# Optimization experiments

Measured on AMD Instinct MI355X. Metric: run time of the kernel, lower is better.

The kernel has to match this reference:

```python
import jax, jax.numpy as jnp
import numpy as np

B, N, D = 32, 4096, 1024

def setup_inputs() -> dict:
    key = jax.random.key(0)
    k1, k2, k3, k4 = jax.random.split(key, 4)
    return {
        "x_final": jax.random.normal(k1, (B, D), dtype=jnp.float32),
        "x_full": jax.random.normal(k2, (B, N, D), dtype=jnp.float32),
        "mask": jnp.ones((B, N), dtype=bool),
        "q": jax.random.normal(k3, (D,), dtype=jnp.float32) / np.sqrt(D),
        "head_w": jax.random.normal(k4, (1, D), dtype=jnp.float32) / np.sqrt(D),
        "head_b": jnp.zeros((1,), dtype=jnp.float32),
    }

def reference(x_final, x_full, mask, q, head_w, head_b):
    # x_final is accepted (as in the torch module) but unused.
    d = x_full.shape[-1]
    inv_sqrt_d = 1.0 / np.sqrt(d)
    # logits: [B, N] = matvec of x_full with learned query q
    logits = jnp.einsum('bnd,d->bn', x_full, q) * inv_sqrt_d
    logits = jnp.where(mask, logits, -jnp.inf)
    alpha = jax.nn.softmax(logits, axis=-1)          # [B, N]
    pooled = jnp.einsum('bn,bnd->bd', alpha, x_full) # [B, D]
    scores = (pooled @ head_w.T + head_b)[:, 0]      # [B]
    return scores, alpha
```

## Files before the change

### kernel.cpp

```cpp
#include <hip/hip_runtime.h>
#include <math.h>

#define B_ 32
#define N_ 4096
#define D_ 1024
#define ROWS (B_ * N_)

#define P1_BLOCKS 2048
#define P1_THREADS 256
#define NWAVES (P1_BLOCKS * (P1_THREADS / 64))
#define ROWS_PER_WAVE (ROWS / NWAVES)

typedef float f32x4 __attribute__((ext_vector_type(4)));

__global__ __launch_bounds__(256) void probe_pass1(
    const float* __restrict__ x,
    const float* __restrict__ q,
    const float* __restrict__ w,
    const unsigned char* __restrict__ mask_b,
    const unsigned* __restrict__ mask_i,
    float* __restrict__ logits,
    float* __restrict__ tvals)
{
    const int lane  = threadIdx.x & 63;
    const int gwave = (int)((blockIdx.x * blockDim.x + threadIdx.x) >> 6);
    const int base  = gwave * ROWS_PER_WAVE;

    const bool use_i32 = (__ballot(mask_i[lane] <= 1u) == ~0ull);

    const f32x4* q4 = (const f32x4*)q;
    const f32x4* w4 = (const f32x4*)w;
    f32x4 qv[4], wv[4];
#pragma unroll
    for (int j = 0; j < 4; ++j) {
        qv[j] = q4[j * 64 + lane];
        wv[j] = w4[j * 64 + lane];
    }

    float lq = 0.f, lw = 0.f;

#pragma unroll 4
    for (int i = 0; i < ROWS_PER_WAVE; ++i) {
        const f32x4* xr = (const f32x4*)(x + (size_t)(base + i) * D_);
        f32x4 xv[4];
#pragma unroll
        for (int j = 0; j < 4; ++j)
            xv[j] = __builtin_nontemporal_load(&xr[j * 64 + lane]);

        float aq = 0.f, aw = 0.f;
#pragma unroll
        for (int j = 0; j < 4; ++j) {
            aq += xv[j].x * qv[j].x + xv[j].y * qv[j].y
                + xv[j].z * qv[j].z + xv[j].w * qv[j].w;
            aw += xv[j].x * wv[j].x + xv[j].y * wv[j].y
                + xv[j].z * wv[j].z + xv[j].w * wv[j].w;
        }
#pragma unroll
        for (int off = 32; off; off >>= 1) {
            aq += __shfl_xor(aq, off);
            aw += __shfl_xor(aw, off);
        }
        if (lane == i) { lq = aq; lw = aw; }
    }

    if (lane < ROWS_PER_WAVE) {
        const int row = base + lane;
        const bool m = use_i32 ? (mask_i[row] != 0u) : (mask_b[row] != 0);
        logits[row] = m ? lq * 0.03125f : -INFINITY;
        tvals[row]  = lw;
    }
}

__global__ __launch_bounds__(256) void probe_pass2(
    const float* __restrict__ logits,
    const float* __restrict__ tvals,
    const float* __restrict__ head_b,
    float* __restrict__ out)
{
    const int b    = blockIdx.x;
    const int tid  = threadIdx.x;
    const int lane = tid & 63;
    const int wid  = tid >> 6;

    __shared__ float redmax[4];
    __shared__ float redsum[8];

    const float4* l4 = (const float4*)(logits + (size_t)b * N_);
    const float4* t4 = (const float4*)(tvals  + (size_t)b * N_);

    float4 lv[4], tv[4];
#pragma unroll
    for (int k = 0; k < 4; ++k) {
        lv[k] = l4[k * 256 + tid];
        tv[k] = t4[k * 256 + tid];
    }

    float m = -INFINITY;
#pragma unroll
    for (int k = 0; k < 4; ++k)
        m = fmaxf(m, fmaxf(fmaxf(lv[k].x, lv[k].y), fmaxf(lv[k].z, lv[k].w)));
#pragma unroll
    for (int off = 32; off; off >>= 1) m = fmaxf(m, __shfl_xor(m, off));
    if (lane == 0) redmax[wid] = m;
    __syncthreads();
    m = fmaxf(fmaxf(redmax[0], redmax[1]), fmaxf(redmax[2], redmax[3]));

    float se = 0.f, set = 0.f;
    float4 ev[4];
#pragma unroll
    for (int k = 0; k < 4; ++k) {
        ev[k].x = __expf(lv[k].x - m);
        ev[k].y = __expf(lv[k].y - m);
        ev[k].z = __expf(lv[k].z - m);
        ev[k].w = __expf(lv[k].w - m);
        se  += ev[k].x + ev[k].y + ev[k].z + ev[k].w;
        set += ev[k].x * tv[k].x + ev[k].y * tv[k].y
             + ev[k].z * tv[k].z + ev[k].w * tv[k].w;
    }
#pragma unroll
    for (int off = 32; off; off >>= 1) {
        se  += __shfl_xor(se, off);
        set += __shfl_xor(set, off);
    }
    if (lane == 0) { redsum[wid] = se; redsum[4 + wid] = set; }
    __syncthreads();
    se  = redsum[0] + redsum[1] + redsum[2] + redsum[3];
    set = redsum[4] + redsum[5] + redsum[6] + redsum[7];

    const float inv = 1.0f / se;

    float4* a4 = (float4*)(out + B_ + (size_t)b * N_);
#pragma unroll
    for (int k = 0; k < 4; ++k) {
        float4 a;
        a.x = ev[k].x * inv; a.y = ev[k].y * inv;
        a.z = ev[k].z * inv; a.w = ev[k].w * inv;
        a4[k * 256 + tid] = a;
    }

    if (tid == 0) out[b] = set * inv + head_b[0];
}

extern "C" void kernel_launch(void* const* d_in, const int* in_sizes, int n_in,
                              void* d_out, int out_size, void* d_ws, size_t ws_size,
                              hipStream_t stream) {
    const float* x_full = (const float*)d_in[1];
    const void*  mask   = d_in[2];
    const float* q      = (const float*)d_in[3];
    const float* head_w = (const float*)d_in[4];
    const float* head_b = (const float*)d_in[5];
    float* out = (float*)d_out;

    float* logits = (float*)d_ws;
    float* tvals  = logits + ROWS;

    probe_pass1<<<P1_BLOCKS, P1_THREADS, 0, stream>>>(
        x_full, q, head_w,
        (const unsigned char*)mask, (const unsigned*)mask,
        logits, tvals);

    probe_pass2<<<B_, 256, 0, stream>>>(logits, tvals, head_b, out);
}
```

Baseline: 88.44 us.

## Fuse softmax pass into matvec kernel via per-batch last-block atomic counter

Merges the two kernels into one. Each block increments a per-batch atomic counter after writing its logits and head projections, and the last block to finish for a batch runs the softmax and pooled-score reduction. This removes the second kernel launch and the serialization gap between the kernels. It adds a memset launch to reset the counters, threadfence and atomic overhead, and a serial tail where only 32 blocks do the reduction work.

```diff
diff --git a/kernel.cpp b/kernel.cpp
--- a/kernel.cpp
+++ b/kernel.cpp
@@ -10,17 +10,21 @@
 #define P1_THREADS 256
 #define NWAVES (P1_BLOCKS * (P1_THREADS / 64))
 #define ROWS_PER_WAVE (ROWS / NWAVES)
+#define BLOCKS_PER_BATCH (P1_BLOCKS / B_)
 
 typedef float f32x4 __attribute__((ext_vector_type(4)));
 
-__global__ __launch_bounds__(256) void probe_pass1(
+__global__ __launch_bounds__(256) void probe_fused(
     const float* __restrict__ x,
     const float* __restrict__ q,
     const float* __restrict__ w,
     const unsigned char* __restrict__ mask_b,
     const unsigned* __restrict__ mask_i,
     float* __restrict__ logits,
-    float* __restrict__ tvals)
+    float* __restrict__ tvals,
+    int* __restrict__ counters,
+    const float* __restrict__ head_b,
+    float* __restrict__ out)
 {
     const int lane  = threadIdx.x & 63;
     const int gwave = (int)((blockIdx.x * blockDim.x + threadIdx.x) >> 6);
@@ -69,18 +73,21 @@
         logits[row] = m ? lq * 0.03125f : -INFINITY;
         tvals[row]  = lw;
     }
-}
 
-__global__ __launch_bounds__(256) void probe_pass2(
-    const float* __restrict__ logits,
-    const float* __restrict__ tvals,
-    const float* __restrict__ head_b,
-    float* __restrict__ out)
-{
-    const int b    = blockIdx.x;
+    const int b = (int)(blockIdx.x >> 6);
+    __shared__ int s_old;
+    __syncthreads();
+    if (threadIdx.x == 0) {
+        __threadfence();
+        s_old = atomicAdd(&counters[b], 1);
+    }
+    __syncthreads();
+    if (s_old != BLOCKS_PER_BATCH - 1) return;
+    __threadfence();
+
     const int tid  = threadIdx.x;
-    const int lane = tid & 63;
-    const int wid  = tid >> 6;
+    const int wlane = tid & 63;
+    const int wid   = tid >> 6;
 
     __shared__ float redmax[4];
     __shared__ float redsum[8];
@@ -101,7 +108,7 @@
         m = fmaxf(m, fmaxf(fmaxf(lv[k].x, lv[k].y), fmaxf(lv[k].z, lv[k].w)));
 #pragma unroll
     for (int off = 32; off; off >>= 1) m = fmaxf(m, __shfl_xor(m, off));
-    if (lane == 0) redmax[wid] = m;
+    if (wlane == 0) redmax[wid] = m;
     __syncthreads();
     m = fmaxf(fmaxf(redmax[0], redmax[1]), fmaxf(redmax[2], redmax[3]));
 
@@ -122,7 +129,7 @@
         se  += __shfl_xor(se, off);
         set += __shfl_xor(set, off);
     }
-    if (lane == 0) { redsum[wid] = se; redsum[4 + wid] = set; }
+    if (wlane == 0) { redsum[wid] = se; redsum[4 + wid] = set; }
     __syncthreads();
     se  = redsum[0] + redsum[1] + redsum[2] + redsum[3];
     set = redsum[4] + redsum[5] + redsum[6] + redsum[7];
@@ -151,13 +158,14 @@
     const float* head_b = (const float*)d_in[5];
     float* out = (float*)d_out;
 
-    float* logits = (float*)d_ws;
-    float* tvals  = logits + ROWS;
+    float* logits   = (float*)d_ws;
+    float* tvals    = logits + ROWS;
+    int*   counters = (int*)(tvals + ROWS);
 
-    probe_pass1<<<P1_BLOCKS, P1_THREADS, 0, stream>>>(
+    hipMemsetAsync(counters, 0, B_ * sizeof(int), stream);
+
+    probe_fused<<<P1_BLOCKS, P1_THREADS, 0, stream>>>(
         x_full, q, head_w,
         (const unsigned char*)mask, (const unsigned*)mask,
-        logits, tvals);
-
-    probe_pass2<<<B_, 256, 0, stream>>>(logits, tvals, head_b, out);
+        logits, tvals, counters, head_b, out);
 }
```

Measured after the change: 238.0 us. 169% more time.
